# Kernel optimization log

Hardware: AMD Instinct MI355X
Metric: run time of the kernel (lower is better)

Reference implementation:

```python
import jax, jax.numpy as jnp
import numpy as np


def setup_inputs() -> dict:
    key = jax.random.key(0)
    k1, k2 = jax.random.split(key)
    B, C, H, W = 32, 2, 512, 512
    inp = jax.random.normal(k1, (B, C, H, W), dtype=jnp.float32)
    tgt = jax.random.normal(k2, (B, C, H, W), dtype=jnp.float32)
    return {"input": inp, "target": tgt}


def reference(input, target):
    B, C, H, W = input.shape
    # normalized coordinate grids: (j+1)/W along x, (p+1)/H along y
    xg = jnp.arange(1, W + 1, dtype=input.dtype) / W  # (W,)
    yg = jnp.arange(1, H + 1, dtype=input.dtype) / H  # (H,)
    # softmax over flattened heatmap per (b, c)
    p = jax.nn.softmax(input.reshape(B, C, H * W), axis=-1).reshape(B, C, H, W)
    # soft-argmax coords in normalized units, then scaled to pixels (*W, *H)
    pred_x = jnp.einsum('bchw,w->bc', p, xg) * W
    pred_y = jnp.einsum('bchw,h->bc', p, yg) * H
    # ground truth: hard argmax of target heatmap -> pixel coords
    idx = jnp.argmax(target.reshape(B, C, H * W), axis=-1)
    true_x = (idx % W + 1).astype(input.dtype)   # ((idx%W+1)/W)*W
    true_y = (idx // W + 1).astype(input.dtype)  # ((idx//W+1)/H)*H
    ed = jnp.sqrt((true_x - pred_x) ** 2 + (true_y - pred_y) ** 2)  # (B, C)
    s_i = jnp.sum(ed[:, 0])   # channel 0 -> inferior
    s_s = jnp.sum(ed[:, 1:])  # remaining channels -> superior
    denom = jnp.asarray(B, input.dtype)
    return (s_i / denom, s_s / denom, (s_i + s_s) / denom)
```

## Files before the change

kernel.cpp:

```cpp
#include <hip/hip_runtime.h>
#include <math.h>

constexpr int Wd      = 512;
constexpr int Hd      = 512;
constexpr int HW      = Wd * Hd;
constexpr int NBC     = 64;
constexpr int SPLITS  = 32;
constexpr int CHUNK   = HW / SPLITS;
constexpr int NPART   = NBC * SPLITS;
constexpr int THREADS = 256;
constexpr int F4_PER_T = CHUNK / 4 / THREADS;


__global__ __launch_bounds__(THREADS, 8) void dsnt_pass1(
    const float* __restrict__ inp, const float* __restrict__ tgt,
    float* __restrict__ ws) {
  const int bid   = blockIdx.x;
  const int role  = bid & 1;
  const int sub   = bid >> 1;
  const int bc    = sub >> 5;
  const int split = sub & (SPLITS - 1);
  const int t     = threadIdx.x;
  const int rbase = split * CHUNK;

  __shared__ float sm0[4], sm1[4], sm2[4];
  __shared__ int   smi[4];
  const int wave = t >> 6;

  float* Pl = ws;
  float* Px = ws + NPART;
  float* Py = ws + 2 * NPART;
  float* Pv = ws + 3 * NPART;
  int*   Pi = (int*)(ws + 4 * NPART);

  if (role == 0) {
    const float4* ip4 = (const float4*)(inp + (size_t)bc * HW + (size_t)rbase);
    float4 a[F4_PER_T];
#pragma unroll
    for (int i = 0; i < F4_PER_T; ++i) a[i] = ip4[t + i * THREADS];
    __builtin_amdgcn_sched_barrier(0);

    float lA = 0.f, lB = 0.f, sxA = 0.f, sxB = 0.f, syA = 0.f, syB = 0.f;
#pragma unroll
    for (int i = 0; i < F4_PER_T; ++i) {
      const int r = rbase + (t + i * THREADS) * 4;
      const float yc = (float)((r >> 9) + 1);
      const float x0 = (float)((r & 511) + 1);
      const float e0 = __expf(a[i].x);
      const float e1 = __expf(a[i].y);
      const float e2 = __expf(a[i].z);
      const float e3 = __expf(a[i].w);
      lA += e0 + e2;
      lB += e1 + e3;
      sxA = fmaf(e0, x0,       sxA);  sxA = fmaf(e2, x0 + 2.f, sxA);
      sxB = fmaf(e1, x0 + 1.f, sxB);  sxB = fmaf(e3, x0 + 3.f, sxB);
      syA = fmaf(e0 + e2, yc, syA);
      syB = fmaf(e1 + e3, yc, syB);
    }
    float l = lA + lB, sx = sxA + sxB, sy = syA + syB;

#pragma unroll
    for (int off = 32; off; off >>= 1) {
      l  += __shfl_xor(l, off);
      sx += __shfl_xor(sx, off);
      sy += __shfl_xor(sy, off);
    }
    if ((t & 63) == 0) { sm0[wave] = l; sm1[wave] = sx; sm2[wave] = sy; }
    __syncthreads();
    if (t == 0) {
#pragma unroll
      for (int wv = 1; wv < 4; ++wv) { l += sm0[wv]; sx += sm1[wv]; sy += sm2[wv]; }
      Pl[sub] = l; Px[sub] = sx; Py[sub] = sy;
    }
  } else {
    const float4* tp4 = (const float4*)(tgt + (size_t)bc * HW + (size_t)rbase);
    float4 b[F4_PER_T];
#pragma unroll
    for (int i = 0; i < F4_PER_T; ++i) b[i] = tp4[t + i * THREADS];
    __builtin_amdgcn_sched_barrier(0);

    float tvA = -INFINITY, tvB = -INFINITY;
    int   tiA = 0, tiB = 0;
#pragma unroll
    for (int i = 0; i < F4_PER_T; ++i) {
      const int r = rbase + (t + i * THREADS) * 4;
      if (b[i].x > tvA) { tvA = b[i].x; tiA = r; }
      if (b[i].z > tvA) { tvA = b[i].z; tiA = r + 2; }
      if (b[i].y > tvB) { tvB = b[i].y; tiB = r + 1; }
      if (b[i].w > tvB) { tvB = b[i].w; tiB = r + 3; }
    }
    float tv = tvA; int ti = tiA;
    if (tvB > tv || (tvB == tv && tiB < ti)) { tv = tvB; ti = tiB; }

#pragma unroll
    for (int off = 32; off; off >>= 1) {
      const float tv2 = __shfl_xor(tv, off);
      const int   ti2 = __shfl_xor(ti, off);
      if (tv2 > tv || (tv2 == tv && ti2 < ti)) { tv = tv2; ti = ti2; }
    }
    if ((t & 63) == 0) { sm0[wave] = tv; smi[wave] = ti; }
    __syncthreads();
    if (t == 0) {
#pragma unroll
      for (int wv = 1; wv < 4; ++wv) {
        const float tv2 = sm0[wv];
        const int   ti2 = smi[wv];
        if (tv2 > tv || (tv2 == tv && ti2 < ti)) { tv = tv2; ti = ti2; }
      }
      Pv[sub] = tv; Pi[sub] = ti;
    }
  }
}

__global__ __launch_bounds__(256) void dsnt_pass2(const float* __restrict__ ws,
                                                  float* __restrict__ out) {
  const int t    = threadIdx.x;
  const int bc   = t >> 2;
  const int part = t & 3;
  const float* Pl = ws;
  const float* Px = ws + NPART;
  const float* Py = ws + 2 * NPART;
  const float* Pv = ws + 3 * NPART;
  const int*   Pi = (const int*)(ws + 4 * NPART);

  float l = 0.f, sx = 0.f, sy = 0.f;
  float tv = -INFINITY;
  int   ti = 0x7fffffff;
#pragma unroll
  for (int j = 0; j < 8; ++j) {
    const int p = bc * SPLITS + part * 8 + j;
    l  += Pl[p];
    sx += Px[p];
    sy += Py[p];
    const float v  = Pv[p];
    const int   ix = Pi[p];
    if (v > tv || (v == tv && ix < ti)) { tv = v; ti = ix; }
  }
#pragma unroll
  for (int off = 1; off <= 2; off <<= 1) {
    l  += __shfl_xor(l, off);
    sx += __shfl_xor(sx, off);
    sy += __shfl_xor(sy, off);
    const float tv2 = __shfl_xor(tv, off);
    const int   ti2 = __shfl_xor(ti, off);
    if (tv2 > tv || (tv2 == tv && ti2 < ti)) { tv = tv2; ti = ti2; }
  }

  __shared__ float edArr[NBC];
  if (part == 0) {
    const float predx = sx / l;
    const float predy = sy / l;
    const float truex = (float)((ti & 511) + 1);
    const float truey = (float)((ti >> 9) + 1);
    const float dx = truex - predx, dy = truey - predy;
    edArr[bc] = sqrtf(dx * dx + dy * dy);
  }
  __syncthreads();
  if (t < NBC) {
    const float ed = edArr[t];
    float ei = (t & 1) ? 0.f : ed;
    float es = (t & 1) ? ed : 0.f;
#pragma unroll
    for (int off = 32; off; off >>= 1) {
      ei += __shfl_xor(ei, off);
      es += __shfl_xor(es, off);
    }
    if (t == 0) {
      out[0] = ei * (1.f / 32.f);
      out[1] = es * (1.f / 32.f);
      out[2] = (ei + es) * (1.f / 32.f);
    }
  }
}

extern "C" void kernel_launch(void* const* d_in, const int* in_sizes, int n_in,
                              void* d_out, int out_size, void* d_ws, size_t ws_size,
                              hipStream_t stream) {
  const float* inp = (const float*)d_in[0];
  const float* tgt = (const float*)d_in[1];
  float* out = (float*)d_out;
  float* ws  = (float*)d_ws;

  dsnt_pass1<<<2 * NPART, THREADS, 0, stream>>>(inp, tgt, ws);
  dsnt_pass2<<<1, 256, 0, stream>>>(ws, out);
}
```

Baseline: 147.0 us.

## Stream input and target chunks per wave through an LDS ring with async global_load_lds

Each wavefront now owns one (bc, split) chunk and processes both the softmax-moment sums and the target argmax, instead of separate blocks per role. Data is loaded with global_load_lds into a 16-slot per-wave LDS ring buffer, with vmcnt-based waits keeping 16 loads in flight while earlier slots are consumed. This removes block-level syncs and the register-heavy bulk preload, and is meant to sustain memory throughput with deep prefetch. The trade-off is 64KB of LDS per block, which limits occupancy, plus fragile hand-written waitcnt ordering.

Result: slower. 150.7 us (+2.5%).

```diff
diff --git a/kernel.cpp b/kernel.cpp
--- a/kernel.cpp
+++ b/kernel.cpp
@@ -9,23 +9,28 @@
 constexpr int CHUNK   = HW / SPLITS;
 constexpr int NPART   = NBC * SPLITS;
 constexpr int THREADS = 256;
-constexpr int F4_PER_T = CHUNK / 4 / THREADS;
-
-
-__global__ __launch_bounds__(THREADS, 8) void dsnt_pass1(
+
+typedef float f32x4 __attribute__((ext_vector_type(4)));
+typedef __attribute__((address_space(3))) void       lds_vp;
+typedef const __attribute__((address_space(1))) void gbl_vp;
+
+
+__global__ __launch_bounds__(THREADS) void dsnt_pass1(
     const float* __restrict__ inp, const float* __restrict__ tgt,
     float* __restrict__ ws) {
-  const int bid   = blockIdx.x;
-  const int role  = bid & 1;
-  const int sub   = bid >> 1;
-  const int bc    = sub >> 5;
-  const int split = sub & (SPLITS - 1);
-  const int t     = threadIdx.x;
+  __shared__ alignas(16) char smem[65536];
+
+  const int t    = threadIdx.x;
+  const int wave = t >> 6;
+  const int lane = t & 63;
+  const int w     = (blockIdx.x << 2) | wave;
+  const int bc    = w >> 5;
+  const int split = w & (SPLITS - 1);
   const int rbase = split * CHUNK;
 
-  __shared__ float sm0[4], sm1[4], sm2[4];
-  __shared__ int   smi[4];
-  const int wave = t >> 6;
+  const char* gin = (const char*)(inp + (size_t)bc * HW + (size_t)rbase);
+  const char* gtg = (const char*)(tgt + (size_t)bc * HW + (size_t)rbase);
+  char* ring = smem + (wave << 14);
 
   float* Pl = ws;
   float* Px = ws + NPART;
@@ -33,82 +38,95 @@
   float* Pv = ws + 3 * NPART;
   int*   Pi = (int*)(ws + 4 * NPART);
 
-  if (role == 0) {
-    const float4* ip4 = (const float4*)(inp + (size_t)bc * HW + (size_t)rbase);
-    float4 a[F4_PER_T];
-#pragma unroll
-    for (int i = 0; i < F4_PER_T; ++i) a[i] = ip4[t + i * THREADS];
+#pragma unroll
+  for (int j = 0; j < 16; ++j) {
+    __builtin_amdgcn_global_load_lds(
+        (gbl_vp*)(gin + j * 1024 + lane * 16),
+        (lds_vp*)(ring + ((j & 15) << 10)), 16, 0, 0);
+  }
+
+  float lA = 0.f, lB = 0.f, sxA = 0.f, sxB = 0.f, syA = 0.f, syB = 0.f;
+  float tvA = -INFINITY, tvB = -INFINITY;
+  int   tiA = 0, tiB = 0;
+
+  const f32x4* rp = (const f32x4*)ring;
+
+#pragma unroll
+  for (int k = 0; k < 48; ++k) {
+    asm volatile("s_waitcnt vmcnt(15)" ::: "memory");
     __builtin_amdgcn_sched_barrier(0);
-
-    float lA = 0.f, lB = 0.f, sxA = 0.f, sxB = 0.f, syA = 0.f, syB = 0.f;
-#pragma unroll
-    for (int i = 0; i < F4_PER_T; ++i) {
-      const int r = rbase + (t + i * THREADS) * 4;
+    const f32x4 v = rp[((k & 15) << 6) + lane];
+    asm volatile("s_waitcnt lgkmcnt(0)" ::: "memory");
+    __builtin_amdgcn_sched_barrier(0);
+    {
+      const int j = k + 16;
+      const char* g = (j < 32) ? (gin + j * 1024) : (gtg + (j - 32) * 1024);
+      __builtin_amdgcn_global_load_lds(
+          (gbl_vp*)(g + lane * 16),
+          (lds_vp*)(ring + ((j & 15) << 10)), 16, 0, 0);
+    }
+    if (k < 32) {
+      const int r = rbase + (k << 8) + (lane << 2);
       const float yc = (float)((r >> 9) + 1);
       const float x0 = (float)((r & 511) + 1);
-      const float e0 = __expf(a[i].x);
-      const float e1 = __expf(a[i].y);
-      const float e2 = __expf(a[i].z);
-      const float e3 = __expf(a[i].w);
+      const float e0 = __expf(v[0]);
+      const float e1 = __expf(v[1]);
+      const float e2 = __expf(v[2]);
+      const float e3 = __expf(v[3]);
       lA += e0 + e2;
       lB += e1 + e3;
       sxA = fmaf(e0, x0,       sxA);  sxA = fmaf(e2, x0 + 2.f, sxA);
       sxB = fmaf(e1, x0 + 1.f, sxB);  sxB = fmaf(e3, x0 + 3.f, sxB);
       syA = fmaf(e0 + e2, yc, syA);
       syB = fmaf(e1 + e3, yc, syB);
-    }
-    float l = lA + lB, sx = sxA + sxB, sy = syA + syB;
-
-#pragma unroll
-    for (int off = 32; off; off >>= 1) {
-      l  += __shfl_xor(l, off);
-      sx += __shfl_xor(sx, off);
-      sy += __shfl_xor(sy, off);
-    }
-    if ((t & 63) == 0) { sm0[wave] = l; sm1[wave] = sx; sm2[wave] = sy; }
-    __syncthreads();
-    if (t == 0) {
-#pragma unroll
-      for (int wv = 1; wv < 4; ++wv) { l += sm0[wv]; sx += sm1[wv]; sy += sm2[wv]; }
-      Pl[sub] = l; Px[sub] = sx; Py[sub] = sy;
-    }
-  } else {
-    const float4* tp4 = (const float4*)(tgt + (size_t)bc * HW + (size_t)rbase);
-    float4 b[F4_PER_T];
-#pragma unroll
-    for (int i = 0; i < F4_PER_T; ++i) b[i] = tp4[t + i * THREADS];
-    __builtin_amdgcn_sched_barrier(0);
-
-    float tvA = -INFINITY, tvB = -INFINITY;
-    int   tiA = 0, tiB = 0;
-#pragma unroll
-    for (int i = 0; i < F4_PER_T; ++i) {
-      const int r = rbase + (t + i * THREADS) * 4;
-      if (b[i].x > tvA) { tvA = b[i].x; tiA = r; }
-      if (b[i].z > tvA) { tvA = b[i].z; tiA = r + 2; }
-      if (b[i].y > tvB) { tvB = b[i].y; tiB = r + 1; }
-      if (b[i].w > tvB) { tvB = b[i].w; tiB = r + 3; }
-    }
-    float tv = tvA; int ti = tiA;
-    if (tvB > tv || (tvB == tv && tiB < ti)) { tv = tvB; ti = tiB; }
-
-#pragma unroll
-    for (int off = 32; off; off >>= 1) {
-      const float tv2 = __shfl_xor(tv, off);
-      const int   ti2 = __shfl_xor(ti, off);
-      if (tv2 > tv || (tv2 == tv && ti2 < ti)) { tv = tv2; ti = ti2; }
-    }
-    if ((t & 63) == 0) { sm0[wave] = tv; smi[wave] = ti; }
-    __syncthreads();
-    if (t == 0) {
-#pragma unroll
-      for (int wv = 1; wv < 4; ++wv) {
-        const float tv2 = sm0[wv];
-        const int   ti2 = smi[wv];
-        if (tv2 > tv || (tv2 == tv && ti2 < ti)) { tv = tv2; ti = ti2; }
-      }
-      Pv[sub] = tv; Pi[sub] = ti;
-    }
+    } else {
+      const int r = rbase + ((k - 32) << 8) + (lane << 2);
+      if (v[0] > tvA) { tvA = v[0]; tiA = r; }
+      if (v[2] > tvA) { tvA = v[2]; tiA = r + 2; }
+      if (v[1] > tvB) { tvB = v[1]; tiB = r + 1; }
+      if (v[3] > tvB) { tvB = v[3]; tiB = r + 3; }
+    }
+  }
+
+  asm volatile("s_waitcnt vmcnt(8)" ::: "memory");
+  __builtin_amdgcn_sched_barrier(0);
+#pragma unroll
+  for (int k = 48; k < 56; ++k) {
+    const f32x4 v = rp[((k & 15) << 6) + lane];
+    const int r = rbase + ((k - 32) << 8) + (lane << 2);
+    if (v[0] > tvA) { tvA = v[0]; tiA = r; }
+    if (v[2] > tvA) { tvA = v[2]; tiA = r + 2; }
+    if (v[1] > tvB) { tvB = v[1]; tiB = r + 1; }
+    if (v[3] > tvB) { tvB = v[3]; tiB = r + 3; }
+  }
+  asm volatile("s_waitcnt vmcnt(0)" ::: "memory");
+  __builtin_amdgcn_sched_barrier(0);
+#pragma unroll
+  for (int k = 56; k < 64; ++k) {
+    const f32x4 v = rp[((k & 15) << 6) + lane];
+    const int r = rbase + ((k - 32) << 8) + (lane << 2);
+    if (v[0] > tvA) { tvA = v[0]; tiA = r; }
+    if (v[2] > tvA) { tvA = v[2]; tiA = r + 2; }
+    if (v[1] > tvB) { tvB = v[1]; tiB = r + 1; }
+    if (v[3] > tvB) { tvB = v[3]; tiB = r + 3; }
+  }
+
+  float l = lA + lB, sx = sxA + sxB, sy = syA + syB;
+  float tv = tvA; int ti = tiA;
+  if (tvB > tv || (tvB == tv && tiB < ti)) { tv = tvB; ti = tiB; }
+
+#pragma unroll
+  for (int off = 32; off; off >>= 1) {
+    l  += __shfl_xor(l, off);
+    sx += __shfl_xor(sx, off);
+    sy += __shfl_xor(sy, off);
+    const float tv2 = __shfl_xor(tv, off);
+    const int   ti2 = __shfl_xor(ti, off);
+    if (tv2 > tv || (tv2 == tv && ti2 < ti)) { tv = tv2; ti = ti2; }
+  }
+  if (lane == 0) {
+    Pl[w] = l; Px[w] = sx; Py[w] = sy;
+    Pv[w] = tv; Pi[w] = ti;
   }
 }
 
@@ -181,6 +199,6 @@
   float* out = (float*)d_out;
   float* ws  = (float*)d_ws;
 
-  dsnt_pass1<<<2 * NPART, THREADS, 0, stream>>>(inp, tgt, ws);
+  dsnt_pass1<<<NPART / 4, THREADS, 0, stream>>>(inp, tgt, ws);
   dsnt_pass2<<<1, 256, 0, stream>>>(ws, out);
 }
```

## Fuse final reduction into pass1 via last-block atomic counter

Applied to the files above, without the earlier changes.

Merges the second reduction kernel into the first: every block increments a global counter after writing its partials, and the last block to arrive reads all partials and computes the final loss values. A memset clears the counter before launch, which replaces the second kernel launch with a memset node. The sched_barrier directives after the loads are also removed, so the compiler is free to interleave loads with computation.

Result: slower. 337.5 us (+129.6%).

```diff
diff --git a/kernel.cpp b/kernel.cpp
--- a/kernel.cpp
+++ b/kernel.cpp
@@ -10,11 +10,12 @@
 constexpr int NPART   = NBC * SPLITS;
 constexpr int THREADS = 256;
 constexpr int F4_PER_T = CHUNK / 4 / THREADS;
+constexpr int NBLK    = 2 * NPART;
 
 
 __global__ __launch_bounds__(THREADS, 8) void dsnt_pass1(
     const float* __restrict__ inp, const float* __restrict__ tgt,
-    float* __restrict__ ws) {
+    float* __restrict__ ws, float* __restrict__ out) {
   const int bid   = blockIdx.x;
   const int role  = bid & 1;
   const int sub   = bid >> 1;
@@ -25,6 +26,7 @@
 
   __shared__ float sm0[4], sm1[4], sm2[4];
   __shared__ int   smi[4];
+  __shared__ bool  lastBlk;
   const int wave = t >> 6;
 
   float* Pl = ws;
@@ -32,13 +34,13 @@
   float* Py = ws + 2 * NPART;
   float* Pv = ws + 3 * NPART;
   int*   Pi = (int*)(ws + 4 * NPART);
+  unsigned int* ctr = (unsigned int*)(ws + 5 * NPART);
 
   if (role == 0) {
     const float4* ip4 = (const float4*)(inp + (size_t)bc * HW + (size_t)rbase);
     float4 a[F4_PER_T];
 #pragma unroll
     for (int i = 0; i < F4_PER_T; ++i) a[i] = ip4[t + i * THREADS];
-    __builtin_amdgcn_sched_barrier(0);
 
     float lA = 0.f, lB = 0.f, sxA = 0.f, sxB = 0.f, syA = 0.f, syB = 0.f;
 #pragma unroll
@@ -77,7 +79,6 @@
     float4 b[F4_PER_T];
 #pragma unroll
     for (int i = 0; i < F4_PER_T; ++i) b[i] = tp4[t + i * THREADS];
-    __builtin_amdgcn_sched_barrier(0);
 
     float tvA = -INFINITY, tvB = -INFINITY;
     int   tiA = 0, tiB = 0;
@@ -110,65 +111,68 @@
       Pv[sub] = tv; Pi[sub] = ti;
     }
   }
-}
 
-__global__ __launch_bounds__(256) void dsnt_pass2(const float* __restrict__ ws,
-                                                  float* __restrict__ out) {
-  const int t    = threadIdx.x;
-  const int bc   = t >> 2;
-  const int part = t & 3;
-  const float* Pl = ws;
-  const float* Px = ws + NPART;
-  const float* Py = ws + 2 * NPART;
-  const float* Pv = ws + 3 * NPART;
-  const int*   Pi = (const int*)(ws + 4 * NPART);
-
-  float l = 0.f, sx = 0.f, sy = 0.f;
-  float tv = -INFINITY;
-  int   ti = 0x7fffffff;
-#pragma unroll
-  for (int j = 0; j < 8; ++j) {
-    const int p = bc * SPLITS + part * 8 + j;
-    l  += Pl[p];
-    sx += Px[p];
-    sy += Py[p];
-    const float v  = Pv[p];
-    const int   ix = Pi[p];
-    if (v > tv || (v == tv && ix < ti)) { tv = v; ti = ix; }
-  }
-#pragma unroll
-  for (int off = 1; off <= 2; off <<= 1) {
-    l  += __shfl_xor(l, off);
-    sx += __shfl_xor(sx, off);
-    sy += __shfl_xor(sy, off);
-    const float tv2 = __shfl_xor(tv, off);
-    const int   ti2 = __shfl_xor(ti, off);
-    if (tv2 > tv || (tv2 == tv && ti2 < ti)) { tv = tv2; ti = ti2; }
-  }
-
-  __shared__ float edArr[NBC];
-  if (part == 0) {
-    const float predx = sx / l;
-    const float predy = sy / l;
-    const float truex = (float)((ti & 511) + 1);
-    const float truey = (float)((ti >> 9) + 1);
-    const float dx = truex - predx, dy = truey - predy;
-    edArr[bc] = sqrtf(dx * dx + dy * dy);
+  __syncthreads();
+  if (t == 0) {
+    __threadfence();
+    const unsigned int old = atomicAdd(ctr, 1u);
+    lastBlk = (old == (unsigned int)(NBLK - 1));
   }
   __syncthreads();
-  if (t < NBC) {
-    const float ed = edArr[t];
-    float ei = (t & 1) ? 0.f : ed;
-    float es = (t & 1) ? ed : 0.f;
+  if (!lastBlk) return;
+  __threadfence();
+
+  {
+    const int bc2  = t >> 2;
+    const int part = t & 3;
+
+    float l = 0.f, sx = 0.f, sy = 0.f;
+    float tv = -INFINITY;
+    int   ti = 0x7fffffff;
 #pragma unroll
-    for (int off = 32; off; off >>= 1) {
-      ei += __shfl_xor(ei, off);
-      es += __shfl_xor(es, off);
+    for (int j = 0; j < 8; ++j) {
+      const int p = bc2 * SPLITS + part * 8 + j;
+      l  += Pl[p];
+      sx += Px[p];
+      sy += Py[p];
+      const float v  = Pv[p];
+      const int   ix = Pi[p];
+      if (v > tv || (v == tv && ix < ti)) { tv = v; ti = ix; }
     }
-    if (t == 0) {
-      out[0] = ei * (1.f / 32.f);
-      out[1] = es * (1.f / 32.f);
-      out[2] = (ei + es) * (1.f / 32.f);
+#pragma unroll
+    for (int off = 1; off <= 2; off <<= 1) {
+      l  += __shfl_xor(l, off);
+      sx += __shfl_xor(sx, off);
+      sy += __shfl_xor(sy, off);
+      const float tv2 = __shfl_xor(tv, off);
+      const int   ti2 = __shfl_xor(ti, off);
+      if (tv2 > tv || (tv2 == tv && ti2 < ti)) { tv = tv2; ti = ti2; }
+    }
+
+    __shared__ float edArr[NBC];
+    if (part == 0) {
+      const float predx = sx / l;
+      const float predy = sy / l;
+      const float truex = (float)((ti & 511) + 1);
+      const float truey = (float)((ti >> 9) + 1);
+      const float dx = truex - predx, dy = truey - predy;
+      edArr[bc2] = sqrtf(dx * dx + dy * dy);
+    }
+    __syncthreads();
+    if (t < NBC) {
+      const float ed = edArr[t];
+      float ei = (t & 1) ? 0.f : ed;
+      float es = (t & 1) ? ed : 0.f;
+#pragma unroll
+      for (int off = 32; off; off >>= 1) {
+        ei += __shfl_xor(ei, off);
+        es += __shfl_xor(es, off);
+      }
+      if (t == 0) {
+        out[0] = ei * (1.f / 32.f);
+        out[1] = es * (1.f / 32.f);
+        out[2] = (ei + es) * (1.f / 32.f);
+      }
     }
   }
 }
@@ -181,6 +185,6 @@
   float* out = (float*)d_out;
   float* ws  = (float*)d_ws;
 
-  dsnt_pass1<<<2 * NPART, THREADS, 0, stream>>>(inp, tgt, ws);
-  dsnt_pass2<<<1, 256, 0, stream>>>(ws, out);
+  (void)hipMemsetAsync(ws + 5 * NPART, 0, sizeof(unsigned int), stream);
+  dsnt_pass1<<<NBLK, THREADS, 0, stream>>>(inp, tgt, ws, out);
 }
```
